# Performance work log

Measured on AMD Instinct MI355X. Metric: run time of the kernel, lower is better.

The kernel has to match this reference:

```python
import jax, jax.numpy as jnp
import numpy as np

B, SWIN_D, VIT_D, E, H = 16384, 768, 512, 1024, 4
HD = E // H  # 256


def setup_inputs() -> dict:
    key = jax.random.key(0)
    ks = jax.random.split(key, 12)
    s = lambda fan_in: 1.0 / np.sqrt(fan_in)
    return {
        "swin_feat": jax.random.normal(ks[0], (B, SWIN_D), jnp.float32),
        "vit_feat": jax.random.normal(ks[1], (B, VIT_D), jnp.float32),
        # outer projections (nn.Linear: y = x @ W.T + b)
        "Wq": jax.random.uniform(ks[2], (E, SWIN_D), jnp.float32, -s(SWIN_D), s(SWIN_D)),
        "bq": jax.random.uniform(ks[3], (E,), jnp.float32, -s(SWIN_D), s(SWIN_D)),
        "Wk": jax.random.uniform(ks[4], (E, VIT_D), jnp.float32, -s(VIT_D), s(VIT_D)),
        "bk": jax.random.uniform(ks[5], (E,), jnp.float32, -s(VIT_D), s(VIT_D)),
        "Wv": jax.random.uniform(ks[6], (E, VIT_D), jnp.float32, -s(VIT_D), s(VIT_D)),
        "bv": jax.random.uniform(ks[7], (E,), jnp.float32, -s(VIT_D), s(VIT_D)),
        # nn.MultiheadAttention internal in_proj (stacked q,k,v) and out_proj
        "in_proj_w": jax.random.uniform(ks[8], (3 * E, E), jnp.float32, -s(E), s(E)),
        "in_proj_b": jnp.zeros((3 * E,), jnp.float32),
        "Wo": jax.random.uniform(ks[9], (E, E), jnp.float32, -s(E), s(E)),
        "bo": jnp.zeros((E,), jnp.float32),
    }


def reference(swin_feat, vit_feat, Wq, bq, Wk, bk, Wv, bv, in_proj_w, in_proj_b, Wo, bo):
    # outer projections -> [B, E] (seq_len = 1, so the seq dim is implicit)
    q = swin_feat @ Wq.T + bq
    k = vit_feat @ Wk.T + bk
    v = vit_feat @ Wv.T + bv
    # MultiheadAttention in-projection (split stacked weight)
    Wiq, Wik, Wiv = in_proj_w[:E], in_proj_w[E:2 * E], in_proj_w[2 * E:]
    biq, bik, biv = in_proj_b[:E], in_proj_b[E:2 * E], in_proj_b[2 * E:]
    q2 = (q @ Wiq.T + biq).reshape(B, H, HD)
    k2 = (k @ Wik.T + bik).reshape(B, H, HD)
    v2 = (v @ Wiv.T + biv).reshape(B, H, HD)
    # attention with q_len = kv_len = 1
    scale = 1.0 / np.sqrt(HD)
    scores = jnp.einsum('bhd,bhd->bh', q2, k2) * scale        # [B, H]
    w = jax.nn.softmax(scores[..., None], axis=-1)             # softmax over 1 key -> ones
    attn = w * v2                                              # [B, H, HD]
    out = attn.reshape(B, E) @ Wo.T + bo                       # out-projection
    return out
```

## Files before the change

### kernel.cpp

```cpp
#include <hip/hip_runtime.h>
#include <stdint.h>
#include <stddef.h>

#define E_DIM 1024

typedef __bf16 v8bf __attribute__((ext_vector_type(8)));
typedef float v4f __attribute__((ext_vector_type(4)));

__device__ __forceinline__ unsigned short f2bf(float x) {
  unsigned int u = __builtin_bit_cast(unsigned int, x);
  u += 0x7fffu + ((u >> 16) & 1u);
  return (unsigned short)(u >> 16);
}

template <int RB>
__device__ __forceinline__ int swz(int r, int c) {
  if constexpr (RB >= 128) return c ^ ((r & 7) << 4);
  else return c;
}

template <int N>
__device__ __forceinline__ void waitcnt_vm() {
  static_assert(N == 0 || N == 4 || N == 8 || N == 12, "add literal");
  if constexpr (N == 0)  asm volatile("s_waitcnt vmcnt(0)" ::: "memory");
  if constexpr (N == 4)  asm volatile("s_waitcnt vmcnt(4)" ::: "memory");
  if constexpr (N == 8)  asm volatile("s_waitcnt vmcnt(8)" ::: "memory");
  if constexpr (N == 12) asm volatile("s_waitcnt vmcnt(12)" ::: "memory");
}

template <int ROWS, int BK>
__device__ __forceinline__ void stageg(const unsigned short* __restrict__ G, int g0,
                                       int ldg, int k0, char* L, int wid, int lane) {
  constexpr int RB = BK * 2;
  constexpr int ITERS = (ROWS * RB) / 4096;
#pragma unroll
  for (int it = 0; it < ITERS; ++it) {
    int lbase = it * 4096 + wid * 1024;
    int lin = lbase + lane * 16;
    int r = lin / RB, cb = lin % RB;
    int gcb = swz<RB>(r, cb);
    const char* g = (const char*)G + ((size_t)(g0 + r) * ldg + k0) * 2 + gcb;
    __builtin_amdgcn_global_load_lds((const __attribute__((address_space(1))) void*)g,
                                     (__attribute__((address_space(3))) void*)(L + lbase),
                                     16, 0, 0);
  }
}

template <int RB>
__device__ __forceinline__ v8bf frag_bf16(const char* L, int r, int kelem) {
  int o = swz<RB>(r, kelem * 2);
  return *(const v8bf*)(L + r * RB + o);
}

template <int BM, int BN, int BK, int FM, int FN>
__device__ __forceinline__ void compute_tile(const char* Al, const char* Bl,
                                             v4f (&acc)[FM][FN],
                                             int wr, int wc, int lr, int kg) {
  constexpr int RBA = BK * 2, RBB = BK * 2;
  constexpr int TMW = BM / 2, TNW = BN / 2;
#pragma unroll
  for (int kk = 0; kk < BK / 32; ++kk) {
    const int ke = kk * 32 + kg * 8;
    v8bf a[FM], b[FN];
#pragma unroll
    for (int mi = 0; mi < FM; ++mi)
      a[mi] = frag_bf16<RBA>(Al, wr * TMW + mi * 16 + lr, ke);
#pragma unroll
    for (int ni = 0; ni < FN; ++ni)
      b[ni] = frag_bf16<RBB>(Bl, wc * TNW + ni * 16 + lr, ke);
#pragma unroll
    for (int mi = 0; mi < FM; ++mi)
#pragma unroll
      for (int ni = 0; ni < FN; ++ni)
        acc[mi][ni] = __builtin_amdgcn_mfma_f32_16x16x32_bf16(a[mi], b[ni], acc[mi][ni], 0, 0, 0);
  }
}

__device__ __forceinline__ void cvt4(const float4* __restrict__ src,
                                     ushort4* __restrict__ dst, int i0) {
#pragma unroll
  for (int j = 0; j < 4; ++j) {
    int i = i0 + j * 256;
    float4 f = src[i];
    ushort4 u;
    u.x = f2bf(f.x); u.y = f2bf(f.y); u.z = f2bf(f.z); u.w = f2bf(f.w);
    dst[i] = u;
  }
}

__device__ __forceinline__ void mv4(const float* __restrict__ W, const float* __restrict__ x,
                                    const float* __restrict__ b, float* __restrict__ y,
                                    int blkrel, int tid) {
  int r = blkrel * 4 + (tid >> 6);
  int lane = tid & 63;
  float s = 0.f;
  for (int c = lane; c < 1024; c += 64) s += W[(size_t)r * 1024 + c] * x[c];
#pragma unroll
  for (int off = 32; off; off >>= 1) s += __shfl_down(s, off);
  if (lane == 0) y[r] = s + b[r];
}

__global__ __launch_bounds__(256) void prep1(const float* __restrict__ Wv,
                                             unsigned short* __restrict__ WvT,
                                             const float* __restrict__ Wiv,
                                             const float* __restrict__ bv,
                                             const float* __restrict__ biv,
                                             float* __restrict__ b1,
                                             unsigned short* __restrict__ Wivb) {
  int bid = blockIdx.x;
  int tid = threadIdx.x;
  if (bid < 512) {
    __shared__ float tile[32][33];
    const int R = 1024, C = 512;
    int nbx = C >> 5;
    int bx = bid % nbx, by = bid / nbx;
    int tx = tid & 31, ty = tid >> 5;
#pragma unroll
    for (int i = 0; i < 32; i += 8)
      tile[ty + i][tx] = Wv[(size_t)(by * 32 + ty + i) * C + bx * 32 + tx];
    __syncthreads();
#pragma unroll
    for (int i = 0; i < 32; i += 8)
      WvT[(size_t)(bx * 32 + ty + i) * R + by * 32 + tx] = f2bf(tile[tx][ty + i]);
  } else if (bid < 768) {
    mv4(Wiv, bv, biv, b1, bid - 512, tid);
  } else {
    cvt4((const float4*)Wiv, (ushort4*)Wivb, (bid - 768) * 1024 + tid);
  }
}

template <int BM, int BN, int BK, int FM, int FN, int OUTBF, int XCDSWZ>
__global__ __launch_bounds__(256) void gemm_cv(const unsigned short* __restrict__ A,
                                               const unsigned short* __restrict__ B,
                                               const float* __restrict__ bias,
                                               float* __restrict__ Cf,
                                               unsigned short* __restrict__ Cb,
                                               int M, int N, int K,
                                               const float* __restrict__ mvW,
                                               const float* __restrict__ mvx,
                                               const float* __restrict__ mvb,
                                               float* __restrict__ mvy, int nmv,
                                               const float* __restrict__ csrc1,
                                               unsigned short* __restrict__ cdst1,
                                               int cbase1, int ncv1,
                                               const float* __restrict__ csrc2,
                                               unsigned short* __restrict__ cdst2,
                                               int cbase2) {
  static_assert((BM + BN) * BK * 2 / 1024 / 4 == 4, "vmcnt literals assume 4 loads/tile/wave");
  __shared__ __align__(16) char Al0[BM * BK * 2];
  __shared__ __align__(16) char Al1[BM * BK * 2];
  __shared__ __align__(16) char Al2[BM * BK * 2];
  __shared__ __align__(16) char Al3[BM * BK * 2];
  __shared__ __align__(16) char Bl0[BN * BK * 2];
  __shared__ __align__(16) char Bl1[BN * BK * 2];
  __shared__ __align__(16) char Bl2[BN * BK * 2];
  __shared__ __align__(16) char Bl3[BN * BK * 2];
  const int nbn = N / BN;
  const int ngemm = nbn * (M / BM);
  int bid = blockIdx.x;
  const int tid = threadIdx.x;

  if (bid >= ngemm) {
    int rel = bid - ngemm;
    if (rel < nmv) {
      mv4(mvW, mvx, mvb, mvy, rel, tid);
    } else if (rel < nmv + ncv1) {
      cvt4((const float4*)csrc1, (ushort4*)cdst1, (cbase1 + rel - nmv) * 1024 + tid);
    } else {
      cvt4((const float4*)csrc2, (ushort4*)cdst2, (cbase2 + rel - nmv - ncv1) * 1024 + tid);
    }
    return;
  }

  int bm_i, bn_i;
  if (XCDSWZ) {
    int x = bid & 7, j = bid >> 3;
    bm_i = x + ((j >> 3) << 3);
    bn_i = j & 7;
  } else {
    bm_i = bid / nbn;
    bn_i = bid % nbn;
  }
  const int bm0 = bm_i * BM, bn0 = bn_i * BN;

  constexpr int TMW = BM / 2, TNW = BN / 2;
  const int lane = tid & 63;
  const int wid = tid >> 6;
  const int wr = wid >> 1, wc = wid & 1;
  const int lr = lane & 15;
  const int kg = lane >> 4;

  v4f acc[FM][FN];
#pragma unroll
  for (int i = 0; i < FM; ++i)
#pragma unroll
    for (int j = 0; j < FN; ++j) acc[i][j] = 0.f;

  const int NT = K / BK;

  stageg<BM, BK>(A, bm0, K, 0 * BK, Al0, wid, lane);
  stageg<BN, BK>(B, bn0, K, 0 * BK, Bl0, wid, lane);
  stageg<BM, BK>(A, bm0, K, 1 * BK, Al1, wid, lane);
  stageg<BN, BK>(B, bn0, K, 1 * BK, Bl1, wid, lane);
  stageg<BM, BK>(A, bm0, K, 2 * BK, Al2, wid, lane);
  stageg<BN, BK>(B, bn0, K, 2 * BK, Bl2, wid, lane);

#define GEMM_PHASE(CA, CB, SA, SB, TNXT, W)                              \
  waitcnt_vm<W>();                                                       \
  __builtin_amdgcn_s_barrier();                                          \
  __builtin_amdgcn_sched_barrier(0);                                     \
  if ((TNXT) < NT) {                                                     \
    stageg<BM, BK>(A, bm0, K, (TNXT)*BK, SA, wid, lane);                 \
    stageg<BN, BK>(B, bn0, K, (TNXT)*BK, SB, wid, lane);                 \
  }                                                                      \
  __builtin_amdgcn_s_setprio(1);                                         \
  compute_tile<BM, BN, BK, FM, FN>(CA, CB, acc, wr, wc, lr, kg);         \
  __builtin_amdgcn_s_setprio(0);                                         \
  __builtin_amdgcn_sched_barrier(0);

  for (int t = 0; t + 8 <= NT; t += 4) {
    GEMM_PHASE(Al0, Bl0, Al3, Bl3, t + 3, 8)
    GEMM_PHASE(Al1, Bl1, Al0, Bl0, t + 4, 8)
    GEMM_PHASE(Al2, Bl2, Al1, Bl1, t + 5, 8)
    GEMM_PHASE(Al3, Bl3, Al2, Bl2, t + 6, 8)
  }
  GEMM_PHASE(Al0, Bl0, Al3, Bl3, NT - 1, 8)
  GEMM_PHASE(Al1, Bl1, Al0, Bl0, NT, 8)
  GEMM_PHASE(Al2, Bl2, Al1, Bl1, NT, 4)
  GEMM_PHASE(Al3, Bl3, Al2, Bl2, NT, 0)
#undef GEMM_PHASE

#pragma unroll
  for (int ni = 0; ni < FN; ++ni) {
    int col = bn0 + wc * TNW + ni * 16 + lr;
    float bz = bias ? bias[col] : 0.f;
#pragma unroll
    for (int mi = 0; mi < FM; ++mi) {
      int row0 = bm0 + wr * TMW + mi * 16 + kg * 4;
#pragma unroll
      for (int r = 0; r < 4; ++r) {
        float v = acc[mi][ni][r] + bz;
        if (OUTBF) Cb[(size_t)(row0 + r) * N + col] = f2bf(v);
        else       Cf[(size_t)(row0 + r) * N + col] = v;
      }
    }
  }
}

__global__ __launch_bounds__(256) void gemm_k4(const unsigned short* __restrict__ A,
                                               const unsigned short* __restrict__ B,
                                               const float* __restrict__ bias,
                                               float* __restrict__ C,
                                               int M, int N, int K) {
  __shared__ __align__(16) char Al0[128 * 128];
  __shared__ __align__(16) char Al1[128 * 128];
  __shared__ __align__(16) char Bl0[128 * 128];
  __shared__ __align__(16) char Bl1[128 * 128];
  const int tid = threadIdx.x;
  const int lane = tid & 63, wid = tid >> 6;
  const int wr = wid >> 1, wc = wid & 1;
  const int lr = lane & 15, kg = lane >> 4;

  int bid = blockIdx.x;
  int x = bid & 7, j = bid >> 3;
  const int bm0 = (x + ((j >> 3) << 3)) * 128;
  const int bn0 = (j & 7) * 128;

  v4f acc[4][4];
#pragma unroll
  for (int i = 0; i < 4; ++i)
#pragma unroll
    for (int jj = 0; jj < 4; ++jj) acc[i][jj] = 0.f;

  stageg<128, 64>(A, bm0, K, 0, Al0, wid, lane);
  stageg<128, 64>(B, bn0, K, 0, Bl0, wid, lane);
  stageg<128, 64>(A, bm0, K, 64, Al1, wid, lane);
  stageg<128, 64>(B, bn0, K, 64, Bl1, wid, lane);

#define K4P(CA, CB, TN2, W)                                              \
  waitcnt_vm<W>();                                                       \
  __builtin_amdgcn_s_barrier();                                          \
  __builtin_amdgcn_sched_barrier(0);                                     \
  __builtin_amdgcn_s_setprio(1);                                         \
  compute_tile<128, 128, 64, 4, 4>(CA, CB, acc, wr, wc, lr, kg);         \
  __builtin_amdgcn_s_setprio(0);                                         \
  __builtin_amdgcn_sched_barrier(0);                                     \
  __builtin_amdgcn_s_barrier();                                          \
  if constexpr ((TN2) < 8) {                                             \
    stageg<128, 64>(A, bm0, K, (TN2)*64, CA, wid, lane);                 \
    stageg<128, 64>(B, bn0, K, (TN2)*64, CB, wid, lane);                 \
  }

  K4P(Al0, Bl0, 2, 8)
  K4P(Al1, Bl1, 3, 8)
  K4P(Al0, Bl0, 4, 8)
  K4P(Al1, Bl1, 5, 8)
  K4P(Al0, Bl0, 6, 8)
  K4P(Al1, Bl1, 7, 8)
  K4P(Al0, Bl0, 8, 8)
  K4P(Al1, Bl1, 8, 0)
#undef K4P

#pragma unroll
  for (int ni = 0; ni < 4; ++ni) {
    int col = bn0 + wc * 64 + ni * 16 + lr;
    float bz = bias[col];
#pragma unroll
    for (int mi = 0; mi < 4; ++mi) {
      int row0 = bm0 + wr * 64 + mi * 16 + kg * 4;
#pragma unroll
      for (int r = 0; r < 4; ++r)
        C[(size_t)(row0 + r) * N + col] = acc[mi][ni][r] + bz;
    }
  }
}

extern "C" void kernel_launch(void* const* d_in, const int* in_sizes, int n_in,
                              void* d_out, int out_size, void* d_ws, size_t ws_size,
                              hipStream_t stream) {
  const float* vit = (const float*)d_in[1];
  const float* Wv  = (const float*)d_in[6];
  const float* bv  = (const float*)d_in[7];
  const float* ipw = (const float*)d_in[8];
  const float* ipb = (const float*)d_in[9];
  const float* Wo  = (const float*)d_in[10];
  const float* bo  = (const float*)d_in[11];
  const float* Wiv = ipw + 2 * E_DIM * E_DIM;
  const float* biv = ipb + 2 * E_DIM;

  char* ws = (char*)d_ws;
  unsigned short* Xb   = (unsigned short*)(ws);
  unsigned short* Wivb = (unsigned short*)(ws + (16 << 20));
  unsigned short* Wob  = (unsigned short*)(ws + (18 << 20));
  unsigned short* WvTb = (unsigned short*)(ws + (20 << 20));
  unsigned short* Ttb  = (unsigned short*)(ws + (21 << 20));
  unsigned short* Wcb  = (unsigned short*)(ws + (22 << 20));
  float* b1 = (float*)(ws + (23 << 20));
  float* bc = (float*)(ws + (23 << 20) + 4096);

  prep1<<<1024, 256, 0, stream>>>(Wv, WvTb, Wiv, bv, biv, b1, Wivb);

  gemm_cv<64, 64, 64, 2, 2, 1, 0><<<128 + 256 + 256 + 2048, 256, 0, stream>>>(
      WvTb, Wivb, nullptr, nullptr, Ttb, 512, 1024, 1024,
      Wo, b1, bo, bc, 256,
      Wo, Wob, 0, 256,
      vit, Xb, 0);

  gemm_cv<64, 64, 64, 2, 2, 1, 0><<<128, 256, 0, stream>>>(
      Wob, Ttb, nullptr, nullptr, Wcb, 1024, 512, 1024,
      nullptr, nullptr, nullptr, nullptr, 0,
      nullptr, nullptr, 0, 0,
      nullptr, nullptr, 0);

  gemm_k4<<<1024, 256, 0, stream>>>(Xb, Wcb, bc, (float*)d_out, 16384, 1024, 512);
}
```

Before: 57.06 us.

## Fuse fp32-to-bf16 weight conversion and transpose into weight-folding GEMM loads

Replaces the separate prep kernel (transpose and convert Wv, convert Wiv) and the bf16 staging of Wo with GEMMs that load fp32 weights directly, converting them to bf16 in registers and writing swizzled LDS tiles (transposed for Wv). This cuts the launch chain from four kernels to three and removes the intermediate bf16 weight buffers and their global round trips. In exchange the GEMMs use a simpler register-staged double buffer instead of the four-deep async pipeline. The transposed LDS write is scalar 16-bit stores, which may cause bank conflicts.

```diff
diff --git a/kernel.cpp b/kernel.cpp
--- a/kernel.cpp
+++ b/kernel.cpp
@@ -76,6 +76,41 @@
   }
 }
 
+__device__ __forceinline__ void ldf32(const float* __restrict__ G, int g0, int ldg,
+                                      int c0, int tid, float4 (&r)[4]) {
+#pragma unroll
+  for (int p = 0; p < 4; ++p) {
+    int i4 = p * 256 + tid;
+    int row = i4 >> 4, c4 = i4 & 15;
+    r[p] = *(const float4*)(G + (size_t)(g0 + row) * ldg + c0 + c4 * 4);
+  }
+}
+
+__device__ __forceinline__ void wrf32(const float4 (&r)[4], char* L, int tid) {
+#pragma unroll
+  for (int p = 0; p < 4; ++p) {
+    int i4 = p * 256 + tid;
+    int row = i4 >> 4, c4 = i4 & 15;
+    ushort4 u;
+    u.x = f2bf(r[p].x); u.y = f2bf(r[p].y); u.z = f2bf(r[p].z); u.w = f2bf(r[p].w);
+    *(ushort4*)(L + row * 128 + swz<128>(row, c4 * 8)) = u;
+  }
+}
+
+__device__ __forceinline__ void wrf32T(const float4 (&r)[4], char* L, int tid) {
+#pragma unroll
+  for (int p = 0; p < 4; ++p) {
+    int i4 = p * 256 + tid;
+    int kk = i4 >> 4, c4 = i4 & 15;
+    const float* f = (const float*)&r[p];
+#pragma unroll
+    for (int j = 0; j < 4; ++j) {
+      int m = c4 * 4 + j;
+      *(unsigned short*)(L + m * 128 + swz<128>(m, kk * 2)) = f2bf(f[j]);
+    }
+  }
+}
+
 __device__ __forceinline__ void cvt4(const float4* __restrict__ src,
                                      ushort4* __restrict__ dst, int i0) {
 #pragma unroll
@@ -100,149 +135,135 @@
   if (lane == 0) y[r] = s + b[r];
 }
 
-__global__ __launch_bounds__(256) void prep1(const float* __restrict__ Wv,
-                                             unsigned short* __restrict__ WvT,
-                                             const float* __restrict__ Wiv,
-                                             const float* __restrict__ bv,
-                                             const float* __restrict__ biv,
-                                             float* __restrict__ b1,
-                                             unsigned short* __restrict__ Wivb) {
-  int bid = blockIdx.x;
-  int tid = threadIdx.x;
-  if (bid < 512) {
-    __shared__ float tile[32][33];
-    const int R = 1024, C = 512;
-    int nbx = C >> 5;
-    int bx = bid % nbx, by = bid / nbx;
-    int tx = tid & 31, ty = tid >> 5;
-#pragma unroll
-    for (int i = 0; i < 32; i += 8)
-      tile[ty + i][tx] = Wv[(size_t)(by * 32 + ty + i) * C + bx * 32 + tx];
+__global__ __launch_bounds__(256) void k2_fused(const float* __restrict__ Wv,
+                                                const float* __restrict__ Wiv,
+                                                const float* __restrict__ bv,
+                                                const float* __restrict__ biv,
+                                                float* __restrict__ b1,
+                                                unsigned short* __restrict__ Tt,
+                                                const float* __restrict__ vit,
+                                                unsigned short* __restrict__ Xb) {
+  int bid = blockIdx.x, tid = threadIdx.x;
+  if (bid >= 128) {
+    int rel = bid - 128;
+    if (rel < 256) mv4(Wiv, bv, biv, b1, rel, tid);
+    else cvt4((const float4*)vit, (ushort4*)Xb, (rel - 256) * 1024 + tid);
+    return;
+  }
+  __shared__ __align__(16) char Al0[64 * 128];
+  __shared__ __align__(16) char Al1[64 * 128];
+  __shared__ __align__(16) char Bl0[64 * 128];
+  __shared__ __align__(16) char Bl1[64 * 128];
+  const int bm0 = (bid >> 4) * 64, bn0 = (bid & 15) * 64;
+  const int lane = tid & 63, wid = tid >> 6;
+  const int wr = wid >> 1, wc = wid & 1, lr = lane & 15, kg = lane >> 4;
+
+  v4f acc[2][2];
+#pragma unroll
+  for (int i = 0; i < 2; ++i)
+#pragma unroll
+    for (int j = 0; j < 2; ++j) acc[i][j] = 0.f;
+
+  float4 ra[4], rb[4];
+  ldf32(Wv, 0, 512, bm0, tid, ra);
+  ldf32(Wiv, bn0, 1024, 0, tid, rb);
+  wrf32T(ra, Al0, tid);
+  wrf32(rb, Bl0, tid);
+  __syncthreads();
+
+  for (int t = 0; t < 16; t += 2) {
+    ldf32(Wv, (t + 1) * 64, 512, bm0, tid, ra);
+    ldf32(Wiv, bn0, 1024, (t + 1) * 64, tid, rb);
+    __builtin_amdgcn_sched_barrier(0);
+    compute_tile<64, 64, 64, 2, 2>(Al0, Bl0, acc, wr, wc, lr, kg);
+    wrf32T(ra, Al1, tid);
+    wrf32(rb, Bl1, tid);
     __syncthreads();
-#pragma unroll
-    for (int i = 0; i < 32; i += 8)
-      WvT[(size_t)(bx * 32 + ty + i) * R + by * 32 + tx] = f2bf(tile[tx][ty + i]);
-  } else if (bid < 768) {
-    mv4(Wiv, bv, biv, b1, bid - 512, tid);
-  } else {
-    cvt4((const float4*)Wiv, (ushort4*)Wivb, (bid - 768) * 1024 + tid);
-  }
-}
-
-template <int BM, int BN, int BK, int FM, int FN, int OUTBF, int XCDSWZ>
-__global__ __launch_bounds__(256) void gemm_cv(const unsigned short* __restrict__ A,
-                                               const unsigned short* __restrict__ B,
-                                               const float* __restrict__ bias,
-                                               float* __restrict__ Cf,
-                                               unsigned short* __restrict__ Cb,
-                                               int M, int N, int K,
-                                               const float* __restrict__ mvW,
-                                               const float* __restrict__ mvx,
-                                               const float* __restrict__ mvb,
-                                               float* __restrict__ mvy, int nmv,
-                                               const float* __restrict__ csrc1,
-                                               unsigned short* __restrict__ cdst1,
-                                               int cbase1, int ncv1,
-                                               const float* __restrict__ csrc2,
-                                               unsigned short* __restrict__ cdst2,
-                                               int cbase2) {
-  static_assert((BM + BN) * BK * 2 / 1024 / 4 == 4, "vmcnt literals assume 4 loads/tile/wave");
-  __shared__ __align__(16) char Al0[BM * BK * 2];
-  __shared__ __align__(16) char Al1[BM * BK * 2];
-  __shared__ __align__(16) char Al2[BM * BK * 2];
-  __shared__ __align__(16) char Al3[BM * BK * 2];
-  __shared__ __align__(16) char Bl0[BN * BK * 2];
-  __shared__ __align__(16) char Bl1[BN * BK * 2];
-  __shared__ __align__(16) char Bl2[BN * BK * 2];
-  __shared__ __align__(16) char Bl3[BN * BK * 2];
-  const int nbn = N / BN;
-  const int ngemm = nbn * (M / BM);
-  int bid = blockIdx.x;
-  const int tid = threadIdx.x;
-
-  if (bid >= ngemm) {
-    int rel = bid - ngemm;
-    if (rel < nmv) {
-      mv4(mvW, mvx, mvb, mvy, rel, tid);
-    } else if (rel < nmv + ncv1) {
-      cvt4((const float4*)csrc1, (ushort4*)cdst1, (cbase1 + rel - nmv) * 1024 + tid);
-    } else {
-      cvt4((const float4*)csrc2, (ushort4*)cdst2, (cbase2 + rel - nmv - ncv1) * 1024 + tid);
-    }
+
+    if (t + 2 < 16) {
+      ldf32(Wv, (t + 2) * 64, 512, bm0, tid, ra);
+      ldf32(Wiv, bn0, 1024, (t + 2) * 64, tid, rb);
+    }
+    __builtin_amdgcn_sched_barrier(0);
+    compute_tile<64, 64, 64, 2, 2>(Al1, Bl1, acc, wr, wc, lr, kg);
+    if (t + 2 < 16) {
+      wrf32T(ra, Al0, tid);
+      wrf32(rb, Bl0, tid);
+    }
+    __syncthreads();
+  }
+
+#pragma unroll
+  for (int ni = 0; ni < 2; ++ni) {
+    int col = bn0 + wc * 32 + ni * 16 + lr;
+#pragma unroll
+    for (int mi = 0; mi < 2; ++mi) {
+      int row0 = bm0 + wr * 32 + mi * 16 + kg * 4;
+#pragma unroll
+      for (int r = 0; r < 4; ++r)
+        Tt[(size_t)(row0 + r) * 1024 + col] = f2bf(acc[mi][ni][r]);
+    }
+  }
+}
+
+__global__ __launch_bounds__(256) void k3_fused(const float* __restrict__ Wo,
+                                                const unsigned short* __restrict__ Tt,
+                                                const float* __restrict__ b1,
+                                                const float* __restrict__ bo,
+                                                float* __restrict__ bc,
+                                                unsigned short* __restrict__ Wc) {
+  int bid = blockIdx.x, tid = threadIdx.x;
+  if (bid >= 128) {
+    mv4(Wo, b1, bo, bc, bid - 128, tid);
     return;
   }
-
-  int bm_i, bn_i;
-  if (XCDSWZ) {
-    int x = bid & 7, j = bid >> 3;
-    bm_i = x + ((j >> 3) << 3);
-    bn_i = j & 7;
-  } else {
-    bm_i = bid / nbn;
-    bn_i = bid % nbn;
-  }
-  const int bm0 = bm_i * BM, bn0 = bn_i * BN;
-
-  constexpr int TMW = BM / 2, TNW = BN / 2;
-  const int lane = tid & 63;
-  const int wid = tid >> 6;
-  const int wr = wid >> 1, wc = wid & 1;
-  const int lr = lane & 15;
-  const int kg = lane >> 4;
-
-  v4f acc[FM][FN];
-#pragma unroll
-  for (int i = 0; i < FM; ++i)
-#pragma unroll
-    for (int j = 0; j < FN; ++j) acc[i][j] = 0.f;
-
-  const int NT = K / BK;
-
-  stageg<BM, BK>(A, bm0, K, 0 * BK, Al0, wid, lane);
-  stageg<BN, BK>(B, bn0, K, 0 * BK, Bl0, wid, lane);
-  stageg<BM, BK>(A, bm0, K, 1 * BK, Al1, wid, lane);
-  stageg<BN, BK>(B, bn0, K, 1 * BK, Bl1, wid, lane);
-  stageg<BM, BK>(A, bm0, K, 2 * BK, Al2, wid, lane);
-  stageg<BN, BK>(B, bn0, K, 2 * BK, Bl2, wid, lane);
-
-#define GEMM_PHASE(CA, CB, SA, SB, TNXT, W)                              \
-  waitcnt_vm<W>();                                                       \
-  __builtin_amdgcn_s_barrier();                                          \
-  __builtin_amdgcn_sched_barrier(0);                                     \
-  if ((TNXT) < NT) {                                                     \
-    stageg<BM, BK>(A, bm0, K, (TNXT)*BK, SA, wid, lane);                 \
-    stageg<BN, BK>(B, bn0, K, (TNXT)*BK, SB, wid, lane);                 \
-  }                                                                      \
-  __builtin_amdgcn_s_setprio(1);                                         \
-  compute_tile<BM, BN, BK, FM, FN>(CA, CB, acc, wr, wc, lr, kg);         \
-  __builtin_amdgcn_s_setprio(0);                                         \
-  __builtin_amdgcn_sched_barrier(0);
-
-  for (int t = 0; t + 8 <= NT; t += 4) {
-    GEMM_PHASE(Al0, Bl0, Al3, Bl3, t + 3, 8)
-    GEMM_PHASE(Al1, Bl1, Al0, Bl0, t + 4, 8)
-    GEMM_PHASE(Al2, Bl2, Al1, Bl1, t + 5, 8)
-    GEMM_PHASE(Al3, Bl3, Al2, Bl2, t + 6, 8)
-  }
-  GEMM_PHASE(Al0, Bl0, Al3, Bl3, NT - 1, 8)
-  GEMM_PHASE(Al1, Bl1, Al0, Bl0, NT, 8)
-  GEMM_PHASE(Al2, Bl2, Al1, Bl1, NT, 4)
-  GEMM_PHASE(Al3, Bl3, Al2, Bl2, NT, 0)
-#undef GEMM_PHASE
-
-#pragma unroll
-  for (int ni = 0; ni < FN; ++ni) {
-    int col = bn0 + wc * TNW + ni * 16 + lr;
-    float bz = bias ? bias[col] : 0.f;
-#pragma unroll
-    for (int mi = 0; mi < FM; ++mi) {
-      int row0 = bm0 + wr * TMW + mi * 16 + kg * 4;
-#pragma unroll
-      for (int r = 0; r < 4; ++r) {
-        float v = acc[mi][ni][r] + bz;
-        if (OUTBF) Cb[(size_t)(row0 + r) * N + col] = f2bf(v);
-        else       Cf[(size_t)(row0 + r) * N + col] = v;
-      }
+  __shared__ __align__(16) char Al0[64 * 128];
+  __shared__ __align__(16) char Al1[64 * 128];
+  __shared__ __align__(16) char Bl0[64 * 128];
+  __shared__ __align__(16) char Bl1[64 * 128];
+  const int bm0 = (bid >> 3) * 64, bn0 = (bid & 7) * 64;
+  const int lane = tid & 63, wid = tid >> 6;
+  const int wr = wid >> 1, wc = wid & 1, lr = lane & 15, kg = lane >> 4;
+
+  v4f acc[2][2];
+#pragma unroll
+  for (int i = 0; i < 2; ++i)
+#pragma unroll
+    for (int j = 0; j < 2; ++j) acc[i][j] = 0.f;
+
+  float4 ra[4];
+  ldf32(Wo, bm0, 1024, 0, tid, ra);
+  stageg<64, 64>(Tt, bn0, 1024, 0, Bl0, wid, lane);
+  wrf32(ra, Al0, tid);
+  __syncthreads();
+
+  for (int t = 0; t < 16; t += 2) {
+    ldf32(Wo, bm0, 1024, (t + 1) * 64, tid, ra);
+    stageg<64, 64>(Tt, bn0, 1024, (t + 1) * 64, Bl1, wid, lane);
+    __builtin_amdgcn_sched_barrier(0);
+    compute_tile<64, 64, 64, 2, 2>(Al0, Bl0, acc, wr, wc, lr, kg);
+    wrf32(ra, Al1, tid);
+    __syncthreads();
+
+    if (t + 2 < 16) {
+      ldf32(Wo, bm0, 1024, (t + 2) * 64, tid, ra);
+      stageg<64, 64>(Tt, bn0, 1024, (t + 2) * 64, Bl0, wid, lane);
+    }
+    __builtin_amdgcn_sched_barrier(0);
+    compute_tile<64, 64, 64, 2, 2>(Al1, Bl1, acc, wr, wc, lr, kg);
+    if (t + 2 < 16) wrf32(ra, Al0, tid);
+    __syncthreads();
+  }
+
+#pragma unroll
+  for (int ni = 0; ni < 2; ++ni) {
+    int col = bn0 + wc * 32 + ni * 16 + lr;
+#pragma unroll
+    for (int mi = 0; mi < 2; ++mi) {
+      int row0 = bm0 + wr * 32 + mi * 16 + kg * 4;
+#pragma unroll
+      for (int r = 0; r < 4; ++r)
+        Wc[(size_t)(row0 + r) * 512 + col] = f2bf(acc[mi][ni][r]);
     }
   }
 }
@@ -329,28 +350,15 @@
   const float* biv = ipb + 2 * E_DIM;
 
   char* ws = (char*)d_ws;
-  unsigned short* Xb   = (unsigned short*)(ws);
-  unsigned short* Wivb = (unsigned short*)(ws + (16 << 20));
-  unsigned short* Wob  = (unsigned short*)(ws + (18 << 20));
-  unsigned short* WvTb = (unsigned short*)(ws + (20 << 20));
-  unsigned short* Ttb  = (unsigned short*)(ws + (21 << 20));
-  unsigned short* Wcb  = (unsigned short*)(ws + (22 << 20));
-  float* b1 = (float*)(ws + (23 << 20));
-  float* bc = (float*)(ws + (23 << 20) + 4096);
-
-  prep1<<<1024, 256, 0, stream>>>(Wv, WvTb, Wiv, bv, biv, b1, Wivb);
-
-  gemm_cv<64, 64, 64, 2, 2, 1, 0><<<128 + 256 + 256 + 2048, 256, 0, stream>>>(
-      WvTb, Wivb, nullptr, nullptr, Ttb, 512, 1024, 1024,
-      Wo, b1, bo, bc, 256,
-      Wo, Wob, 0, 256,
-      vit, Xb, 0);
-
-  gemm_cv<64, 64, 64, 2, 2, 1, 0><<<128, 256, 0, stream>>>(
-      Wob, Ttb, nullptr, nullptr, Wcb, 1024, 512, 1024,
-      nullptr, nullptr, nullptr, nullptr, 0,
-      nullptr, nullptr, 0, 0,
-      nullptr, nullptr, 0);
+  unsigned short* Xb  = (unsigned short*)(ws);
+  unsigned short* Ttb = (unsigned short*)(ws + (16 << 20));
+  unsigned short* Wcb = (unsigned short*)(ws + (17 << 20));
+  float* b1 = (float*)(ws + (18 << 20));
+  float* bc = (float*)(ws + (18 << 20) + 4096);
+
+  k2_fused<<<2432, 256, 0, stream>>>(Wv, Wiv, bv, biv, b1, Ttb, vit, Xb);
+
+  k3_fused<<<384, 256, 0, stream>>>(Wo, Ttb, b1, bo, bc, Wcb);
 
   gemm_k4<<<1024, 256, 0, stream>>>(Xb, Wcb, bc, (float*)d_out, 16384, 1024, 512);
 }
```

After: 61.79 us. +8.3%, slower.

## Fuse fp32-to-bf16 activation conversion into final GEMM's A-tile loading

Applied to the files above, without the earlier changes.

The separate pass that converted vit_feat from fp32 to bf16 into a workspace buffer (2048 extra blocks in the second launch) is removed. The final GEMM now loads fp32 A tiles into registers, converts them to bf16 and writes them swizzled into LDS, software-pipelined against the async B loads with adjusted vmcnt waits. This avoids writing and re-reading a 16 MB intermediate, but it doubles A global read bytes per tile and adds register pressure and VALU conversion work inside the main loop.

```diff
diff --git a/kernel.cpp b/kernel.cpp
--- a/kernel.cpp
+++ b/kernel.cpp
@@ -21,11 +21,12 @@
 
 template <int N>
 __device__ __forceinline__ void waitcnt_vm() {
-  static_assert(N == 0 || N == 4 || N == 8 || N == 12, "add literal");
+  static_assert(N == 0 || N == 4 || N == 8 || N == 12 || N == 16, "add literal");
   if constexpr (N == 0)  asm volatile("s_waitcnt vmcnt(0)" ::: "memory");
   if constexpr (N == 4)  asm volatile("s_waitcnt vmcnt(4)" ::: "memory");
   if constexpr (N == 8)  asm volatile("s_waitcnt vmcnt(8)" ::: "memory");
   if constexpr (N == 12) asm volatile("s_waitcnt vmcnt(12)" ::: "memory");
+  if constexpr (N == 16) asm volatile("s_waitcnt vmcnt(16)" ::: "memory");
 }
 
 template <int ROWS, int BK>
@@ -98,6 +99,27 @@
 #pragma unroll
   for (int off = 32; off; off >>= 1) s += __shfl_down(s, off);
   if (lane == 0) y[r] = s + b[r];
+}
+
+__device__ __forceinline__ void lda_k4(const float* __restrict__ A, int bm0, int k0,
+                                       int tid, float4 (&r)[8]) {
+#pragma unroll
+  for (int p = 0; p < 8; ++p) {
+    int i4 = p * 256 + tid;
+    int row = i4 >> 4, c4 = i4 & 15;
+    r[p] = *(const float4*)(A + (size_t)(bm0 + row) * 512 + k0 + c4 * 4);
+  }
+}
+
+__device__ __forceinline__ void wra_k4(const float4 (&r)[8], char* L, int tid) {
+#pragma unroll
+  for (int p = 0; p < 8; ++p) {
+    int i4 = p * 256 + tid;
+    int row = i4 >> 4, c4 = i4 & 15;
+    ushort4 u;
+    u.x = f2bf(r[p].x); u.y = f2bf(r[p].y); u.z = f2bf(r[p].z); u.w = f2bf(r[p].w);
+    *(ushort4*)(L + row * 128 + swz<128>(row, c4 * 8)) = u;
+  }
 }
 
 __global__ __launch_bounds__(256) void prep1(const float* __restrict__ Wv,
@@ -247,11 +269,11 @@
   }
 }
 
-__global__ __launch_bounds__(256) void gemm_k4(const unsigned short* __restrict__ A,
-                                               const unsigned short* __restrict__ B,
-                                               const float* __restrict__ bias,
-                                               float* __restrict__ C,
-                                               int M, int N, int K) {
+__global__ __launch_bounds__(256) void gemm_k4f(const float* __restrict__ A,
+                                                const unsigned short* __restrict__ B,
+                                                const float* __restrict__ bias,
+                                                float* __restrict__ C) {
+  constexpr int N = 1024;
   __shared__ __align__(16) char Al0[128 * 128];
   __shared__ __align__(16) char Al1[128 * 128];
   __shared__ __align__(16) char Bl0[128 * 128];
@@ -272,13 +294,18 @@
 #pragma unroll
     for (int jj = 0; jj < 4; ++jj) acc[i][jj] = 0.f;
 
-  stageg<128, 64>(A, bm0, K, 0, Al0, wid, lane);
-  stageg<128, 64>(B, bn0, K, 0, Bl0, wid, lane);
-  stageg<128, 64>(A, bm0, K, 64, Al1, wid, lane);
-  stageg<128, 64>(B, bn0, K, 64, Bl1, wid, lane);
-
-#define K4P(CA, CB, TN2, W)                                              \
-  waitcnt_vm<W>();                                                       \
+  float4 ra[8], rb[8];
+
+  lda_k4(A, bm0, 0, tid, ra);
+  stageg<128, 64>(B, bn0, 512, 0, Bl0, wid, lane);
+  lda_k4(A, bm0, 64, tid, rb);
+  stageg<128, 64>(B, bn0, 512, 64, Bl1, wid, lane);
+  waitcnt_vm<16>();
+  wra_k4(ra, Al0, tid);
+  waitcnt_vm<12>();
+
+#define K4FP(CA, CB, RS, RW, AW, TN2, W)                                 \
+  asm volatile("s_waitcnt lgkmcnt(0)" ::: "memory");                     \
   __builtin_amdgcn_s_barrier();                                          \
   __builtin_amdgcn_sched_barrier(0);                                     \
   __builtin_amdgcn_s_setprio(1);                                         \
@@ -287,19 +314,28 @@
   __builtin_amdgcn_sched_barrier(0);                                     \
   __builtin_amdgcn_s_barrier();                                          \
   if constexpr ((TN2) < 8) {                                             \
-    stageg<128, 64>(A, bm0, K, (TN2)*64, CA, wid, lane);                 \
-    stageg<128, 64>(B, bn0, K, (TN2)*64, CB, wid, lane);                 \
-  }
-
-  K4P(Al0, Bl0, 2, 8)
-  K4P(Al1, Bl1, 3, 8)
-  K4P(Al0, Bl0, 4, 8)
-  K4P(Al1, Bl1, 5, 8)
-  K4P(Al0, Bl0, 6, 8)
-  K4P(Al1, Bl1, 7, 8)
-  K4P(Al0, Bl0, 8, 8)
-  K4P(Al1, Bl1, 8, 0)
-#undef K4P
+    lda_k4(A, bm0, (TN2)*64, tid, RS);                                   \
+    stageg<128, 64>(B, bn0, 512, (TN2)*64, CB, wid, lane);               \
+  }                                                                      \
+  if constexpr ((TN2) <= 8) {                                            \
+    waitcnt_vm<((TN2) < 8) ? 12 : 0>();                                  \
+    wra_k4(RW, AW, tid);                                                 \
+  }                                                                      \
+  __builtin_amdgcn_sched_barrier(0);
+
+  K4FP(Al0, Bl0, ra, rb, Al1, 2, 12)
+  K4FP(Al1, Bl1, rb, ra, Al0, 3, 12)
+  K4FP(Al0, Bl0, ra, rb, Al1, 4, 12)
+  K4FP(Al1, Bl1, rb, ra, Al0, 5, 12)
+  K4FP(Al0, Bl0, ra, rb, Al1, 6, 12)
+  K4FP(Al1, Bl1, rb, ra, Al0, 7, 12)
+  K4FP(Al0, Bl0, ra, rb, Al1, 8, 0)
+  asm volatile("s_waitcnt lgkmcnt(0)" ::: "memory");
+  __builtin_amdgcn_s_barrier();
+  __builtin_amdgcn_s_setprio(1);
+  compute_tile<128, 128, 64, 4, 4>(Al1, Bl1, acc, wr, wc, lr, kg);
+  __builtin_amdgcn_s_setprio(0);
+#undef K4FP
 
 #pragma unroll
   for (int ni = 0; ni < 4; ++ni) {
@@ -329,22 +365,21 @@
   const float* biv = ipb + 2 * E_DIM;
 
   char* ws = (char*)d_ws;
-  unsigned short* Xb   = (unsigned short*)(ws);
-  unsigned short* Wivb = (unsigned short*)(ws + (16 << 20));
-  unsigned short* Wob  = (unsigned short*)(ws + (18 << 20));
-  unsigned short* WvTb = (unsigned short*)(ws + (20 << 20));
-  unsigned short* Ttb  = (unsigned short*)(ws + (21 << 20));
-  unsigned short* Wcb  = (unsigned short*)(ws + (22 << 20));
-  float* b1 = (float*)(ws + (23 << 20));
-  float* bc = (float*)(ws + (23 << 20) + 4096);
+  unsigned short* Wivb = (unsigned short*)(ws);
+  unsigned short* Wob  = (unsigned short*)(ws + (2 << 20));
+  unsigned short* WvTb = (unsigned short*)(ws + (4 << 20));
+  unsigned short* Ttb  = (unsigned short*)(ws + (5 << 20));
+  unsigned short* Wcb  = (unsigned short*)(ws + (6 << 20));
+  float* b1 = (float*)(ws + (7 << 20));
+  float* bc = (float*)(ws + (7 << 20) + 4096);
 
   prep1<<<1024, 256, 0, stream>>>(Wv, WvTb, Wiv, bv, biv, b1, Wivb);
 
-  gemm_cv<64, 64, 64, 2, 2, 1, 0><<<128 + 256 + 256 + 2048, 256, 0, stream>>>(
+  gemm_cv<64, 64, 64, 2, 2, 1, 0><<<128 + 256 + 256, 256, 0, stream>>>(
       WvTb, Wivb, nullptr, nullptr, Ttb, 512, 1024, 1024,
       Wo, b1, bo, bc, 256,
       Wo, Wob, 0, 256,
-      vit, Xb, 0);
+      nullptr, nullptr, 0);
 
   gemm_cv<64, 64, 64, 2, 2, 1, 0><<<128, 256, 0, stream>>>(
       Wob, Ttb, nullptr, nullptr, Wcb, 1024, 512, 1024,
@@ -352,5 +387,5 @@
       nullptr, nullptr, 0, 0,
       nullptr, nullptr, 0);
 
-  gemm_k4<<<1024, 256, 0, stream>>>(Xb, Wcb, bc, (float*)d_out, 16384, 1024, 512);
-}
+  gemm_k4f<<<1024, 256, 0, stream>>>(vit, Wcb, bc, (float*)d_out);
+}
```

Result: slower. 74.72 us (+30.9%).
